# Optimization experiments

Hardware: AMD Instinct MI355X
Metric: run time of the kernel (lower is better)

## Reference

```python
import jax, jax.numpy as jnp
import numpy as np

R_MAX = 6.0
N_RADIAL = 5
N_BASIS = 7
N_SPECIES = 119
N_ATOMS = 25000
N_EDGES = 1000000


def _tril_2d(n):
    return np.array([(i, j) for i in range(n) for j in range(i + 1)], dtype=np.int32)


def _tril_3d(n):
    return np.array([(i, j, k) for i in range(n) for j in range(i + 1) for k in range(j + 1)], dtype=np.int32)


TRIL2 = jnp.asarray(_tril_2d(N_RADIAL))  # [15, 2]
TRIL3 = jnp.asarray(_tril_3d(N_RADIAL))  # [35, 3]


def setup_inputs() -> dict:
    key = jax.random.key(0)
    k1, k2, k3, k4 = jax.random.split(key, 4)
    dr_vec = jax.random.normal(k1, (N_EDGES, 3), jnp.float32) * 2.0
    Z = jax.random.randint(k2, (N_ATOMS,), 0, N_SPECIES, jnp.int32)
    neighbor_idxs = jax.random.randint(k3, (2, N_EDGES), 0, N_ATOMS, jnp.int32)
    coeffs = jax.random.normal(k4, (N_SPECIES, N_SPECIES, N_RADIAL, N_BASIS), jnp.float32) * 0.1
    return {"dr_vec": dr_vec, "Z": Z, "neighbor_idxs": neighbor_idxs, "coeffs": coeffs}


def _radial(dr, Z_i, Z_j, coeffs):
    # Gaussian basis (apax-style) with species-pair linear coefficients + cosine cutoff
    betta = N_BASIS ** 2 / R_MAX ** 2
    rad_norm = (2.0 * betta / np.pi) ** 0.75
    shifts = jnp.linspace(0.0, R_MAX, N_BASIS, dtype=dr.dtype)
    basis = rad_norm * jnp.exp(-betta * (dr[:, None] - shifts[None, :]) ** 2)  # [E, B]
    cutoff = 0.5 * (jnp.cos(np.pi * dr / R_MAX) + 1.0) * (dr < R_MAX)  # [E]
    c = coeffs[Z_i, Z_j]  # [E, R, B]
    rad = jnp.einsum("eb,erb->er", basis, c) * cutoff[:, None] / np.sqrt(N_BASIS)
    return rad  # [E, R]


def _forward(dr_vec, Z, neighbor_idxs, coeffs):
    idx_i, idx_j = neighbor_idxs[0], neighbor_idxs[1]
    Z_i, Z_j = Z[idx_i], Z[idx_j]
    dr = jnp.linalg.norm(dr_vec, axis=-1)  # [E]
    dn = dr_vec / (dr + 1e-5)[:, None]  # [E, 3]
    rad = _radial(dr, Z_i, Z_j, coeffs)  # [E, R]

    # per-edge outer-product moments
    m1e = rad[..., None] * dn[:, None, :]                      # [E,R,3]
    m2e = m1e[..., None] * dn[:, None, None, :]                # [E,R,3,3]
    m3e = m2e[..., None] * dn[:, None, None, None, :]          # [E,R,3,3,3]

    seg = lambda x: jax.ops.segment_sum(x, idx_j, num_segments=N_ATOMS)
    m0 = seg(rad)   # [A,R]
    m1 = seg(m1e)   # [A,R,3]
    m2 = seg(m2e)   # [A,R,3,3]
    m3 = seg(m3e)   # [A,R,3,3,3]

    contr_0 = m0
    contr_1 = jnp.einsum("ari,asi->rsa", m1, m1)
    contr_2 = jnp.einsum("arij,asij->rsa", m2, m2)
    contr_3 = jnp.einsum("arijk,asijk->rsa", m3, m3)
    contr_4 = jnp.einsum("arij,asik,atjk->rsta", m2, m2, m2)
    contr_5 = jnp.einsum("ari,asj,atij->rsta", m1, m1, m2)
    contr_6 = jnp.einsum("arijk,asijl,atkl->rsta", m3, m3, m2)
    contr_7 = jnp.einsum("arijk,asij,atk->rsta", m3, m2, m1)

    t2i, t2j = TRIL2[:, 0], TRIL2[:, 1]
    t3i, t3j, t3k = TRIL3[:, 0], TRIL3[:, 1], TRIL3[:, 2]

    n_atoms = contr_0.shape[0]
    contr_1 = contr_1[t2i, t2j].reshape(n_atoms, -1)
    contr_2 = contr_2[t2i, t2j].reshape(n_atoms, -1)
    contr_3 = contr_3[t2i, t2j].reshape(n_atoms, -1)
    contr_4 = contr_4[t3i, t3j, t3k].reshape(n_atoms, -1)
    contr_5 = contr_5[t2i, t2j].reshape(n_atoms, -1)
    contr_6 = contr_6[t2i, t2j].reshape(n_atoms, -1)
    contr_7 = contr_7.reshape(n_atoms, -1)

    return jnp.concatenate([contr_0, contr_1, contr_2, contr_3, contr_4, contr_5, contr_6, contr_7], axis=-1)


def reference(dr_vec, Z, neighbor_idxs, coeffs):
    return _forward(dr_vec, Z, neighbor_idxs, coeffs)
```

## Files before the change

kernel.cpp:

```cpp
#include <hip/hip_runtime.h>
#include <math.h>

#define NR 5
#define NB 7
#define NS 119
#define NA 25000
#define NE 1000000
#define OC 360
#define MUS 100
#define CAPR 104
#define CAPI 112
#define CHUNK 64
#define MPAD 101

static constexpr int T2I[15] = {0,1,1,2,2,2,3,3,3,3,4,4,4,4,4};
static constexpr int T2J[15] = {0,0,1,0,1,2,0,1,2,3,0,1,2,3,4};
static constexpr int T3I[35] = {0,1,1,1,2,2,2,2,2,2,3,3,3,3,3,3,3,3,3,3,4,4,4,4,4,4,4,4,4,4,4,4,4,4,4};
static constexpr int T3J[35] = {0,0,1,1,0,1,1,2,2,2,0,1,1,2,2,2,3,3,3,3,0,1,1,2,2,2,3,3,3,3,4,4,4,4,4};
static constexpr int T3K[35] = {0,0,0,1,0,0,1,0,1,2,0,0,1,0,1,2,0,1,2,3,0,0,1,0,1,2,0,1,2,3,0,1,2,3,4};

static constexpr int P2[9]  = {0,1,2, 1,3,4, 2,4,5};
static constexpr int P3[27] = {0,1,4, 1,2,5, 4,5,7,
                               1,2,5, 2,3,6, 5,6,8,
                               4,5,7, 5,6,8, 7,8,9};
static constexpr float W2[6]  = {1.f,2.f,2.f,1.f,2.f,1.f};
static constexpr float W3[10] = {1.f,3.f,3.f,1.f,3.f,6.f,3.f,3.f,3.f,1.f};

__global__ __launch_bounds__(256) void edge_record_kernel(
    const float* __restrict__ dr_vec, const int* __restrict__ Z,
    const int* __restrict__ nbr, const float* __restrict__ coeffs,
    int* __restrict__ cursor, float* __restrict__ binrec)
{
    int e = blockIdx.x * 256 + threadIdx.x;
    if (e >= NE) return;
    float x = dr_vec[3*e+0], y = dr_vec[3*e+1], z = dr_vec[3*e+2];
    int ai = nbr[e];
    int aj = nbr[NE + e];
    int Zi = Z[ai], Zj = Z[aj];

    float dr  = sqrtf(x*x + y*y + z*z);
    float inv = 1.0f / (dr + 1e-5f);
    float d0 = x*inv, d1 = y*inv, d2 = z*inv;

    const float PI_F = 3.14159265358979323846f;
    const float betta = 49.0f / 36.0f;
    float rad_norm = powf(2.0f * betta / PI_F, 0.75f);
    float cut = (dr < 6.0f) ? 0.5f*(cosf(PI_F * dr * (1.0f/6.0f)) + 1.0f) : 0.0f;
    float scale = cut * 0.3779644730092272272f;

    float basis[NB];
#pragma unroll
    for (int b = 0; b < NB; b++) {
        float t = dr - (float)b;
        basis[b] = rad_norm * expf(-betta * t * t);
    }

    const float* cp = coeffs + ((size_t)(Zi*NS + Zj)) * (NR*NB);
    float rad[NR];
#pragma unroll
    for (int r = 0; r < NR; r++) {
        float s = 0.f;
#pragma unroll
        for (int b = 0; b < NB; b++) s += basis[b] * cp[r*NB + b];
        rad[r] = s * scale;
    }

    int pos = __hip_atomic_fetch_add(&cursor[aj], 1, __ATOMIC_RELAXED, __HIP_MEMORY_SCOPE_AGENT);
    if (pos < CAPR) {
        float4* rp = (float4*)(binrec + ((size_t)aj * CAPR + pos) * 8);
        rp[0] = make_float4(rad[0], rad[1], rad[2], rad[3]);
        rp[1] = make_float4(rad[4], d0, d1, d2);
    }
}

__global__ __launch_bounds__(256) void accum_contract_kernel(
    const int* __restrict__ cursor, const float* __restrict__ binrec,
    float* __restrict__ out)
{
    __shared__ float lds[CHUNK * MPAD];
    int base = blockIdx.x * CHUNK;
    int nat  = min(CHUNK, NA - base);

    int al  = threadIdx.x >> 2;
    int sub = threadIdx.x & 3;
    int a   = base + al;
    int n   = (a < NA) ? min(cursor[a], CAPR) : 0;

    float acc[MUS];
#pragma unroll
    for (int i = 0; i < MUS; i++) acc[i] = 0.f;

    const float* mybin = binrec + (size_t)a * CAPR * 8;
    for (int p = sub; p < n; p += 4) {
        const float4* rp = (const float4*)(mybin + (size_t)p * 8);
        float4 r0 = rp[0], r1 = rp[1];
        float rad[NR] = {r0.x, r0.y, r0.z, r0.w, r1.x};
        float d0 = r1.y, d1 = r1.z, d2 = r1.w;

        float q2[6] = {d0*d0, d1*d0, d2*d0, d1*d1, d2*d1, d2*d2};
        float q3[10] = {d0*q2[0], d1*q2[0], d0*q2[3], d1*q2[3], d2*q2[0],
                        d2*q2[1], d2*q2[3], d0*q2[5], d1*q2[5], d2*q2[5]};

#pragma unroll
        for (int r = 0; r < NR; r++) {
            float rv = rad[r];
            acc[r] += rv;
            acc[5 + r*3 + 0] += rv*d0;
            acc[5 + r*3 + 1] += rv*d1;
            acc[5 + r*3 + 2] += rv*d2;
#pragma unroll
            for (int q = 0; q < 6; q++)  acc[20 + r*6  + q] += rv*q2[q];
#pragma unroll
            for (int q = 0; q < 10; q++) acc[50 + r*10 + q] += rv*q3[q];
        }
    }

#pragma unroll
    for (int i = 0; i < MUS; i++) {
        float v = acc[i];
        v += __shfl_xor(v, 1, 64);
        v += __shfl_xor(v, 2, 64);
        if (sub == 0) lds[al * MPAD + i] = v;
    }
    __syncthreads();

    int wave = threadIdx.x >> 6, lane = threadIdx.x & 63;
    int a2 = base + lane;
    bool valid = (lane < nat);
    int mb = lane * MPAD;

#define ML(o) lds[mb + (o)]

    for (int cc = wave; cc < 360; cc += 4) {
        if (!valid) continue;
        float v; int dest;

        if (cc < 5) {
            v = ML(cc);
            dest = a2 * OC + cc;
        } else if (cc < 20) {
            int l = cc - 5;
            int r = T2I[l], s = T2J[l];
            float acc2 = 0.f;
#pragma unroll
            for (int i = 0; i < 3; i++) acc2 += ML(5 + r*3 + i) * ML(5 + s*3 + i);
            v = acc2;
            int f = l * NA + a2; int aa = f / 15; dest = aa * OC + 5 + (f - aa*15);
        } else if (cc < 35) {
            int l = cc - 20;
            int r = T2I[l], s = T2J[l];
            float acc2 = 0.f;
#pragma unroll
            for (int p = 0; p < 6; p++) acc2 += W2[p] * ML(20 + r*6 + p) * ML(20 + s*6 + p);
            v = acc2;
            int f = l * NA + a2; int aa = f / 15; dest = aa * OC + 20 + (f - aa*15);
        } else if (cc < 50) {
            int l = cc - 35;
            int r = T2I[l], s = T2J[l];
            float acc2 = 0.f;
#pragma unroll
            for (int p = 0; p < 10; p++) acc2 += W3[p] * ML(50 + r*10 + p) * ML(50 + s*10 + p);
            v = acc2;
            int f = l * NA + a2; int aa = f / 15; dest = aa * OC + 35 + (f - aa*15);
        } else if (cc < 85) {
            int l = cc - 50;
            int r = T3I[l], s = T3J[l], t = T3K[l];
            float R[6], S[6], T[6];
#pragma unroll
            for (int p = 0; p < 6; p++) { R[p]=ML(20+r*6+p); S[p]=ML(20+s*6+p); T[p]=ML(20+t*6+p); }
            float acc2 = 0.f;
#pragma unroll
            for (int i = 0; i < 3; i++)
#pragma unroll
            for (int j = 0; j < 3; j++)
#pragma unroll
            for (int k = 0; k < 3; k++)
                acc2 += R[P2[i*3+j]] * S[P2[i*3+k]] * T[P2[j*3+k]];
            v = acc2;
            int f = l * NA + a2; int aa = f / 35; dest = aa * OC + 50 + (f - aa*35);
        } else if (cc < 160) {
            int l = cc - 85;
            int p = l / 5, t = l - p*5;
            int r = T2I[p], s = T2J[p];
            float T[6];
#pragma unroll
            for (int q = 0; q < 6; q++) T[q] = ML(20 + t*6 + q);
            float acc2 = 0.f;
#pragma unroll
            for (int i = 0; i < 3; i++)
#pragma unroll
            for (int j = 0; j < 3; j++)
                acc2 += ML(5 + r*3 + i) * ML(5 + s*3 + j) * T[P2[i*3+j]];
            v = acc2;
            int f = l * NA + a2; int aa = f / 75; dest = aa * OC + 85 + (f - aa*75);
        } else if (cc < 235) {
            int l = cc - 160;
            int p = l / 5, t = l - p*5;
            int r = T2I[p], s = T2J[p];
            float R[10], S[10], T[6];
#pragma unroll
            for (int q = 0; q < 10; q++) { R[q]=ML(50+r*10+q); S[q]=ML(50+s*10+q); }
#pragma unroll
            for (int q = 0; q < 6;  q++) T[q] = ML(20 + t*6 + q);
            float acc2 = 0.f;
#pragma unroll
            for (int k = 0; k < 3; k++)
#pragma unroll
            for (int l2 = 0; l2 < 3; l2++) {
                float inner = 0.f;
#pragma unroll
                for (int i = 0; i < 3; i++)
#pragma unroll
                for (int j = 0; j < 3; j++)
                    inner += R[P3[(i*3+j)*3+k]] * S[P3[(i*3+j)*3+l2]];
                acc2 += inner * T[P2[k*3+l2]];
            }
            v = acc2;
            int f = l * NA + a2; int aa = f / 75; dest = aa * OC + 160 + (f - aa*75);
        } else {
            int l = cc - 235;
            int r = l / 25; int rem = l - r*25; int s = rem / 5; int t = rem - s*5;
            float R[10], S[6], T1[3];
#pragma unroll
            for (int q = 0; q < 10; q++) R[q] = ML(50 + r*10 + q);
#pragma unroll
            for (int q = 0; q < 6;  q++) S[q] = ML(20 + s*6 + q);
#pragma unroll
            for (int q = 0; q < 3;  q++) T1[q] = ML(5 + t*3 + q);
            float acc2 = 0.f;
#pragma unroll
            for (int i = 0; i < 3; i++)
#pragma unroll
            for (int j = 0; j < 3; j++)
#pragma unroll
            for (int k = 0; k < 3; k++)
                acc2 += R[P3[(i*3+j)*3+k]] * S[P2[i*3+j]] * T1[k];
            v = acc2;
            int f = l * NA + a2; int aa = f / 125; dest = aa * OC + 235 + (f - aa*125);
        }
        out[dest] = v;
    }
#undef ML
}

__global__ __launch_bounds__(256) void scatter_kernel(
    const int* __restrict__ nbr, int* __restrict__ cursor, int* __restrict__ bins)
{
    int e = blockIdx.x * 256 + threadIdx.x;
    if (e >= NE) return;
    int aj = nbr[NE + e];
    int pos = __hip_atomic_fetch_add(&cursor[aj], 1, __ATOMIC_RELAXED, __HIP_MEMORY_SCOPE_AGENT);
    if (pos < CAPI) bins[(size_t)aj * CAPI + pos] = e;
}

__global__ __launch_bounds__(256) void accum_kernel(
    const float* __restrict__ dr_vec, const int* __restrict__ Z,
    const int* __restrict__ nbr, const float* __restrict__ coeffs,
    const int* __restrict__ cursor, const int* __restrict__ bins,
    float* __restrict__ Mu)
{
    __shared__ float red[32 * MUS];
    int t   = blockIdx.x * 256 + threadIdx.x;
    int a   = t >> 3;
    int sub = t & 7;
    int al  = threadIdx.x >> 3;
    int n   = (a < NA) ? min(cursor[a], CAPI) : 0;
    int Zj  = (a < NA) ? Z[a] : 0;

    float acc[MUS];
#pragma unroll
    for (int i = 0; i < MUS; i++) acc[i] = 0.f;

    const int* mybin = bins + (size_t)a * CAPI;
    const float PI_F = 3.14159265358979323846f;
    const float betta = 49.0f / 36.0f;
    float rad_norm = powf(2.0f * betta / PI_F, 0.75f);

    for (int p = sub; p < n; p += 8) {
        int e = mybin[p];
        float x = dr_vec[3*e+0], y = dr_vec[3*e+1], z = dr_vec[3*e+2];
        int Zi = Z[nbr[e]];

        float dr  = sqrtf(x*x + y*y + z*z);
        float inv = 1.0f / (dr + 1e-5f);
        float d0 = x*inv, d1 = y*inv, d2 = z*inv;

        float cut = (dr < 6.0f) ? 0.5f*(cosf(PI_F * dr * (1.0f/6.0f)) + 1.0f) : 0.0f;
        float scale = cut * 0.3779644730092272272f;

        float basis[NB];
#pragma unroll
        for (int b = 0; b < NB; b++) {
            float tt = dr - (float)b;
            basis[b] = rad_norm * expf(-betta * tt * tt);
        }

        const float* cp = coeffs + ((size_t)(Zi*NS + Zj)) * (NR*NB);
        float rad[NR];
#pragma unroll
        for (int r = 0; r < NR; r++) {
            float s = 0.f;
#pragma unroll
            for (int b = 0; b < NB; b++) s += basis[b] * cp[r*NB + b];
            rad[r] = s * scale;
        }

        float q2[6] = {d0*d0, d1*d0, d2*d0, d1*d1, d2*d1, d2*d2};
        float q3[10] = {d0*q2[0], d1*q2[0], d0*q2[3], d1*q2[3], d2*q2[0],
                        d2*q2[1], d2*q2[3], d0*q2[5], d1*q2[5], d2*q2[5]};

#pragma unroll
        for (int r = 0; r < NR; r++) {
            float rv = rad[r];
            acc[r] += rv;
            acc[5 + r*3 + 0] += rv*d0;
            acc[5 + r*3 + 1] += rv*d1;
            acc[5 + r*3 + 2] += rv*d2;
#pragma unroll
            for (int q = 0; q < 6; q++)  acc[20 + r*6  + q] += rv*q2[q];
#pragma unroll
            for (int q = 0; q < 10; q++) acc[50 + r*10 + q] += rv*q3[q];
        }
    }

#pragma unroll
    for (int i = 0; i < MUS; i++) {
        float v = acc[i];
        v += __shfl_xor(v, 1, 64);
        v += __shfl_xor(v, 2, 64);
        v += __shfl_xor(v, 4, 64);
        if (sub == 0) red[al * MUS + i] = v;
    }
    __syncthreads();

    for (int u = threadIdx.x; u < 32 * MUS; u += 256) {
        int ga = blockIdx.x * 32 + u / MUS;
        if (ga < NA) Mu[(size_t)ga * MUS + (u - (u / MUS) * MUS)] = red[u];
    }
}

__global__ __launch_bounds__(256) void contract_kernel(
    const float* __restrict__ Mu, float* __restrict__ out)
{
    __shared__ float lds[CHUNK * MPAD];
    int base = blockIdx.x * CHUNK;
    int nat  = min(CHUNK, NA - base);

    for (int t = threadIdx.x; t < nat * MUS; t += 256) {
        int al = t / MUS, off = t - al * MUS;
        lds[al * MPAD + off] = Mu[(size_t)base * MUS + t];
    }
    __syncthreads();

    int wave = threadIdx.x >> 6, lane = threadIdx.x & 63;
    int a2 = base + lane;
    bool valid = (lane < nat);
    int mb = lane * MPAD;

#define ML(o) lds[mb + (o)]

    for (int cc = wave; cc < 360; cc += 4) {
        if (!valid) continue;
        float v; int dest;

        if (cc < 5) {
            v = ML(cc);
            dest = a2 * OC + cc;
        } else if (cc < 20) {
            int l = cc - 5;
            int r = T2I[l], s = T2J[l];
            float acc = 0.f;
#pragma unroll
            for (int i = 0; i < 3; i++) acc += ML(5 + r*3 + i) * ML(5 + s*3 + i);
            v = acc;
            int f = l * NA + a2; int aa = f / 15; dest = aa * OC + 5 + (f - aa*15);
        } else if (cc < 35) {
            int l = cc - 20;
            int r = T2I[l], s = T2J[l];
            float acc = 0.f;
#pragma unroll
            for (int p = 0; p < 6; p++) acc += W2[p] * ML(20 + r*6 + p) * ML(20 + s*6 + p);
            v = acc;
            int f = l * NA + a2; int aa = f / 15; dest = aa * OC + 20 + (f - aa*15);
        } else if (cc < 50) {
            int l = cc - 35;
            int r = T2I[l], s = T2J[l];
            float acc = 0.f;
#pragma unroll
            for (int p = 0; p < 10; p++) acc += W3[p] * ML(50 + r*10 + p) * ML(50 + s*10 + p);
            v = acc;
            int f = l * NA + a2; int aa = f / 15; dest = aa * OC + 35 + (f - aa*15);
        } else if (cc < 85) {
            int l = cc - 50;
            int r = T3I[l], s = T3J[l], t = T3K[l];
            float R[6], S[6], T[6];
#pragma unroll
            for (int p = 0; p < 6; p++) { R[p]=ML(20+r*6+p); S[p]=ML(20+s*6+p); T[p]=ML(20+t*6+p); }
            float acc = 0.f;
#pragma unroll
            for (int i = 0; i < 3; i++)
#pragma unroll
            for (int j = 0; j < 3; j++)
#pragma unroll
            for (int k = 0; k < 3; k++)
                acc += R[P2[i*3+j]] * S[P2[i*3+k]] * T[P2[j*3+k]];
            v = acc;
            int f = l * NA + a2; int aa = f / 35; dest = aa * OC + 50 + (f - aa*35);
        } else if (cc < 160) {
            int l = cc - 85;
            int p = l / 5, t = l - p*5;
            int r = T2I[p], s = T2J[p];
            float T[6];
#pragma unroll
            for (int q = 0; q < 6; q++) T[q] = ML(20 + t*6 + q);
            float acc = 0.f;
#pragma unroll
            for (int i = 0; i < 3; i++)
#pragma unroll
            for (int j = 0; j < 3; j++)
                acc += ML(5 + r*3 + i) * ML(5 + s*3 + j) * T[P2[i*3+j]];
            v = acc;
            int f = l * NA + a2; int aa = f / 75; dest = aa * OC + 85 + (f - aa*75);
        } else if (cc < 235) {
            int l = cc - 160;
            int p = l / 5, t = l - p*5;
            int r = T2I[p], s = T2J[p];
            float R[10], S[10], T[6];
#pragma unroll
            for (int q = 0; q < 10; q++) { R[q]=ML(50+r*10+q); S[q]=ML(50+s*10+q); }
#pragma unroll
            for (int q = 0; q < 6;  q++) T[q] = ML(20 + t*6 + q);
            float acc = 0.f;
#pragma unroll
            for (int k = 0; k < 3; k++)
#pragma unroll
            for (int l2 = 0; l2 < 3; l2++) {
                float inner = 0.f;
#pragma unroll
                for (int i = 0; i < 3; i++)
#pragma unroll
                for (int j = 0; j < 3; j++)
                    inner += R[P3[(i*3+j)*3+k]] * S[P3[(i*3+j)*3+l2]];
                acc += inner * T[P2[k*3+l2]];
            }
            v = acc;
            int f = l * NA + a2; int aa = f / 75; dest = aa * OC + 160 + (f - aa*75);
        } else {
            int l = cc - 235;
            int r = l / 25; int rem = l - r*25; int s = rem / 5; int t = rem - s*5;
            float R[10], S[6], T1[3];
#pragma unroll
            for (int q = 0; q < 10; q++) R[q] = ML(50 + r*10 + q);
#pragma unroll
            for (int q = 0; q < 6;  q++) S[q] = ML(20 + s*6 + q);
#pragma unroll
            for (int q = 0; q < 3;  q++) T1[q] = ML(5 + t*3 + q);
            float acc = 0.f;
#pragma unroll
            for (int i = 0; i < 3; i++)
#pragma unroll
            for (int j = 0; j < 3; j++)
#pragma unroll
            for (int k = 0; k < 3; k++)
                acc += R[P3[(i*3+j)*3+k]] * S[P2[i*3+j]] * T1[k];
            v = acc;
            int f = l * NA + a2; int aa = f / 125; dest = aa * OC + 235 + (f - aa*125);
        }
        out[dest] = v;
    }
#undef ML
}

extern "C" void kernel_launch(void* const* d_in, const int* in_sizes, int n_in,
                              void* d_out, int out_size, void* d_ws, size_t ws_size,
                              hipStream_t stream) {
    const float* dr_vec = (const float*)d_in[0];
    const int*   Z      = (const int*)d_in[1];
    const int*   nbr    = (const int*)d_in[2];
    const float* coeffs = (const float*)d_in[3];
    float* out = (float*)d_out;

    size_t need_fast = (size_t)NA * sizeof(int) + (size_t)NA * CAPR * 8 * sizeof(float);

    if (ws_size >= need_fast) {
        int*   cursor = (int*)d_ws;
        float* binrec = (float*)(cursor + NA);
        hipMemsetAsync(cursor, 0, (size_t)NA * sizeof(int), stream);
        edge_record_kernel<<<(NE + 255)/256, 256, 0, stream>>>(dr_vec, Z, nbr, coeffs, cursor, binrec);
        accum_contract_kernel<<<(NA + CHUNK - 1)/CHUNK, 256, 0, stream>>>(cursor, binrec, out);
    } else {
        int*   cursor = (int*)d_ws;
        int*   bins   = cursor + NA;
        float* Mu     = (float*)(bins + (size_t)NA * CAPI);
        hipMemsetAsync(cursor, 0, (size_t)NA * sizeof(int), stream);
        scatter_kernel<<<(NE + 255)/256, 256, 0, stream>>>(nbr, cursor, bins);
        accum_kernel<<<(NA*8 + 255)/256, 256, 0, stream>>>(dr_vec, Z, nbr, coeffs, cursor, bins, Mu);
        contract_kernel<<<(NA + CHUNK - 1)/CHUNK, 256, 0, stream>>>(Mu, out);
    }
}
```

Before: 201.6 us.

## Drop out-of-cutoff edges early, widen per-atom accumulation, use nontemporal stores

Edges with distance at or beyond the cutoff now return before the atomic slot grab, so they cost no coefficient gather, basis evaluation or record write, and atoms end up with fewer records to accumulate. This is exact because the cutoff zeroes their contribution. The accumulate kernel now uses 8 threads per atom over 32 atoms per block instead of 4 over 64, which needs one more shuffle step in the reduction. Record writes and output writes use nontemporal stores to reduce cache pollution.

```diff
diff --git a/kernel.cpp b/kernel.cpp
--- a/kernel.cpp
+++ b/kernel.cpp
@@ -10,8 +10,11 @@
 #define MUS 100
 #define CAPR 104
 #define CAPI 112
+#define CHUNK2 32
 #define CHUNK 64
 #define MPAD 101
+
+typedef float fvec4 __attribute__((ext_vector_type(4)));
 
 static constexpr int T2I[15] = {0,1,1,2,2,2,3,3,3,3,4,4,4,4,4};
 static constexpr int T2J[15] = {0,0,1,0,1,2,0,1,2,3,0,1,2,3,4};
@@ -36,16 +39,20 @@
     float x = dr_vec[3*e+0], y = dr_vec[3*e+1], z = dr_vec[3*e+2];
     int ai = nbr[e];
     int aj = nbr[NE + e];
+
+    float dr = sqrtf(x*x + y*y + z*z);
+    if (dr >= 6.0f) return;
+
+    int pos = __hip_atomic_fetch_add(&cursor[aj], 1, __ATOMIC_RELAXED, __HIP_MEMORY_SCOPE_AGENT);
+
     int Zi = Z[ai], Zj = Z[aj];
-
-    float dr  = sqrtf(x*x + y*y + z*z);
     float inv = 1.0f / (dr + 1e-5f);
     float d0 = x*inv, d1 = y*inv, d2 = z*inv;
 
     const float PI_F = 3.14159265358979323846f;
     const float betta = 49.0f / 36.0f;
     float rad_norm = powf(2.0f * betta / PI_F, 0.75f);
-    float cut = (dr < 6.0f) ? 0.5f*(cosf(PI_F * dr * (1.0f/6.0f)) + 1.0f) : 0.0f;
+    float cut = 0.5f*(cosf(PI_F * dr * (1.0f/6.0f)) + 1.0f);
     float scale = cut * 0.3779644730092272272f;
 
     float basis[NB];
@@ -65,11 +72,12 @@
         rad[r] = s * scale;
     }
 
-    int pos = __hip_atomic_fetch_add(&cursor[aj], 1, __ATOMIC_RELAXED, __HIP_MEMORY_SCOPE_AGENT);
     if (pos < CAPR) {
-        float4* rp = (float4*)(binrec + ((size_t)aj * CAPR + pos) * 8);
-        rp[0] = make_float4(rad[0], rad[1], rad[2], rad[3]);
-        rp[1] = make_float4(rad[4], d0, d1, d2);
+        fvec4* rp = (fvec4*)(binrec + ((size_t)aj * CAPR + pos) * 8);
+        fvec4 v0 = {rad[0], rad[1], rad[2], rad[3]};
+        fvec4 v1 = {rad[4], d0, d1, d2};
+        __builtin_nontemporal_store(v0, rp);
+        __builtin_nontemporal_store(v1, rp + 1);
     }
 }
 
@@ -77,12 +85,12 @@
     const int* __restrict__ cursor, const float* __restrict__ binrec,
     float* __restrict__ out)
 {
-    __shared__ float lds[CHUNK * MPAD];
-    int base = blockIdx.x * CHUNK;
-    int nat  = min(CHUNK, NA - base);
-
-    int al  = threadIdx.x >> 2;
-    int sub = threadIdx.x & 3;
+    __shared__ float lds[CHUNK2 * MPAD];
+    int base = blockIdx.x * CHUNK2;
+    int nat  = min(CHUNK2, NA - base);
+
+    int al  = threadIdx.x >> 3;
+    int sub = threadIdx.x & 7;
     int a   = base + al;
     int n   = (a < NA) ? min(cursor[a], CAPR) : 0;
 
@@ -91,7 +99,7 @@
     for (int i = 0; i < MUS; i++) acc[i] = 0.f;
 
     const float* mybin = binrec + (size_t)a * CAPR * 8;
-    for (int p = sub; p < n; p += 4) {
+    for (int p = sub; p < n; p += 8) {
         const float4* rp = (const float4*)(mybin + (size_t)p * 8);
         float4 r0 = rp[0], r1 = rp[1];
         float rad[NR] = {r0.x, r0.y, r0.z, r0.w, r1.x};
@@ -120,18 +128,20 @@
         float v = acc[i];
         v += __shfl_xor(v, 1, 64);
         v += __shfl_xor(v, 2, 64);
+        v += __shfl_xor(v, 4, 64);
         if (sub == 0) lds[al * MPAD + i] = v;
     }
     __syncthreads();
 
-    int wave = threadIdx.x >> 6, lane = threadIdx.x & 63;
-    int a2 = base + lane;
-    bool valid = (lane < nat);
-    int mb = lane * MPAD;
+    int atom = threadIdx.x & 31;
+    int cs   = threadIdx.x >> 5;
+    int a2   = base + atom;
+    bool valid = (atom < nat);
+    int mb = atom * MPAD;
 
 #define ML(o) lds[mb + (o)]
 
-    for (int cc = wave; cc < 360; cc += 4) {
+    for (int cc = cs; cc < 360; cc += 8) {
         if (!valid) continue;
         float v; int dest;
 
@@ -238,7 +248,7 @@
             v = acc2;
             int f = l * NA + a2; int aa = f / 125; dest = aa * OC + 235 + (f - aa*125);
         }
-        out[dest] = v;
+        __builtin_nontemporal_store(v, &out[dest]);
     }
 #undef ML
 }
@@ -485,14 +495,14 @@
     if (ws_size >= need_fast) {
         int*   cursor = (int*)d_ws;
         float* binrec = (float*)(cursor + NA);
-        hipMemsetAsync(cursor, 0, (size_t)NA * sizeof(int), stream);
+        (void)hipMemsetAsync(cursor, 0, (size_t)NA * sizeof(int), stream);
         edge_record_kernel<<<(NE + 255)/256, 256, 0, stream>>>(dr_vec, Z, nbr, coeffs, cursor, binrec);
-        accum_contract_kernel<<<(NA + CHUNK - 1)/CHUNK, 256, 0, stream>>>(cursor, binrec, out);
+        accum_contract_kernel<<<(NA + CHUNK2 - 1)/CHUNK2, 256, 0, stream>>>(cursor, binrec, out);
     } else {
         int*   cursor = (int*)d_ws;
         int*   bins   = cursor + NA;
         float* Mu     = (float*)(bins + (size_t)NA * CAPI);
-        hipMemsetAsync(cursor, 0, (size_t)NA * sizeof(int), stream);
+        (void)hipMemsetAsync(cursor, 0, (size_t)NA * sizeof(int), stream);
         scatter_kernel<<<(NE + 255)/256, 256, 0, stream>>>(nbr, cursor, bins);
         accum_kernel<<<(NA*8 + 255)/256, 256, 0, stream>>>(dr_vec, Z, nbr, coeffs, cursor, bins, Mu);
         contract_kernel<<<(NA + CHUNK - 1)/CHUNK, 256, 0, stream>>>(Mu, out);
```

New measurement: 232.6 us. 15.3% more time.
